# Kernel optimization log

Measured on AMD Instinct MI355X. Metric: run time of the kernel, lower is better.

## Reference

```python
import jax, jax.numpy as jnp
import numpy as np

B, R, C, OUT, IN = 256, 1152, 10, 16, 8


def setup_inputs() -> dict:
    key = jax.random.key(0)
    kx, kw = jax.random.split(key)
    x = jax.random.normal(kx, (B, R, IN), dtype=jnp.float32)
    W = jax.random.normal(kw, (R, C, OUT, IN), dtype=jnp.float32)
    return {"x": x, "W": W}


def _squash(s):
    # s: [B, C, OUT]
    mag_sq = jnp.sum(s * s, axis=-1, keepdims=True)
    mag = jnp.sqrt(mag_sq + 1e-8)
    return mag_sq / (1.0 + mag_sq) * (s / (mag + 1e-8))


def reference(x, W):
    # u_hat[b,r,c,o] = sum_i W[r,c,o,i] * x[b,r,i]  (no explicit W.repeat)
    u_hat = jnp.einsum('rcoi,bri->brco', W, x)
    b_ij = jnp.zeros((B, R, C), dtype=u_hat.dtype)
    v_j = None
    for it in range(3):
        c_ij = jax.nn.softmax(b_ij, axis=2)              # [B,R,C]
        s_j = jnp.einsum('brc,brco->bco', c_ij, u_hat)   # [B,C,OUT]
        v_j = _squash(s_j)                               # [B,C,OUT]
        if it < 2:
            b_ij = b_ij + jnp.einsum('brco,bco->brc', u_hat, v_j)
    return v_j
```

## Files before the change

kernel.cpp:

```cpp
#include <hip/hip_runtime.h>
#include <math.h>


typedef _Float16 h2 __attribute__((ext_vector_type(2)));
typedef _Float16 h4 __attribute__((ext_vector_type(4)));

#if __has_builtin(__builtin_amdgcn_fdot2)
#define FDOT2(a, b, c) __builtin_amdgcn_fdot2((a), (b), (c), false)
#else
static __device__ __forceinline__ float FDOT2(h2 a, h2 b, float c) {
    return c + (float)a.x * (float)b.x + (float)a.y * (float)b.y;
}
#endif

#if __has_builtin(__builtin_amdgcn_rcpf)
#define FRCP(x) __builtin_amdgcn_rcpf(x)
#else
#define FRCP(x) (1.0f / (x))
#endif

#define BCH2(u) __builtin_bit_cast(h2, (u))

template<int CTRL>
static __device__ __forceinline__ float dpp_xadd(float x) {
    const int t = __builtin_amdgcn_update_dpp(
        0, __builtin_bit_cast(int, x), CTRL, 0xF, 0xF, true);
    return x + __builtin_bit_cast(float, t);
}
static __device__ __forceinline__ float og_allsum(float l) {
    l = dpp_xadd<0xB1>(l);
    l = dpp_xadd<0x4E>(l);
    l = dpp_xadd<0x141>(l);
    return l;
}

namespace {
constexpr int Bdim = 256;
constexpr int Rdim = 1152;
constexpr int Cdim = 10;
constexpr int Odim = 16;
constexpr int Idim = 8;
constexpr int CO   = 160;

constexpr int Rpad  = 1280;
constexpr int RPC   = 10;
constexpr int NPAIR = 5;
constexpr int NCH   = 128;
constexpr int NSP   = 32;
constexpr int WROW  = Cdim * Odim * Idim;
}

__global__ __launch_bounds__(256)
void conv_wx(const float* __restrict__ W, const float* __restrict__ x,
             _Float16* __restrict__ W16, _Float16* __restrict__ X16)
{
    constexpr int NW4 = Rpad * WROW / 4;
    constexpr int NX4 = Rpad * Bdim * Idim / 4;
    const int i = blockIdx.x * 256 + threadIdx.x;
    if (i < NW4) {
        const int r = i / (WROW / 4);
        h4 o = { (_Float16)0.f, (_Float16)0.f, (_Float16)0.f, (_Float16)0.f };
        if (r < Rdim) {
            const float4 v = reinterpret_cast<const float4*>(W)[i];
            o = { (_Float16)v.x, (_Float16)v.y, (_Float16)v.z, (_Float16)v.w };
        }
        reinterpret_cast<h4*>(W16)[i] = o;
    } else if (i < NW4 + NX4) {
        const int j    = i - NW4;
        const int r    = j / (Bdim * 2);
        const int rem  = j - r * (Bdim * 2);
        const int b    = rem >> 1;
        const int half = rem & 1;
        h4 o = { (_Float16)0.f, (_Float16)0.f, (_Float16)0.f, (_Float16)0.f };
        if (r < Rdim) {
            const float4 v = reinterpret_cast<const float4*>(x)
                [((size_t)b * Rdim + r) * 2 + half];
            o = { (_Float16)v.x, (_Float16)v.y, (_Float16)v.z, (_Float16)v.w };
        }
        reinterpret_cast<h4*>(X16)[j] = o;
    }
}

__device__ __forceinline__ void stagepair(const _Float16* __restrict__ src,
                                          _Float16* dst, int lane)
{
#pragma unroll
    for (int k = 0; k < 5; ++k) {
        const _Float16* s = src + (size_t)(k * 64 + lane) * 8;
        _Float16* d = dst + k * 512;
        __builtin_amdgcn_global_load_lds((const __attribute__((address_space(1))) void*)s,
                                         (__attribute__((address_space(3))) void*)d,
                                         16, 0, 0);
    }
}

template<bool FIRST>
__global__ __launch_bounds__(256)
void caps_iter(const _Float16* __restrict__ X16, const _Float16* __restrict__ W16,
               const float* __restrict__ Vsum, float* __restrict__ s_part)
{
    __shared__ __align__(16) _Float16 Wstage[4][2][2560];

    const int tid  = threadIdx.x;
    const int wv   = tid >> 6;
    const int lane = tid & 63;
    const int og   = lane & 7;
    const int bl   = lane >> 3;

    const int quad   = blockIdx.x;
    const int bgroup = blockIdx.y;
    const int chunk  = quad * 4 + wv;
    const int r0     = chunk * RPC;
    const int b0     = bgroup * 16 + bl;
    const int b1     = b0 + 8;

    float va0[Cdim], vb0[Cdim], va1[Cdim], vb1[Cdim];
    if constexpr (!FIRST) {
#pragma unroll
        for (int c = 0; c < Cdim; ++c) {
            const float2 p = *reinterpret_cast<const float2*>(
                Vsum + (size_t)b0 * CO + c * Odim + og * 2);
            va0[c] = p.x; vb0[c] = p.y;
            const float2 q = *reinterpret_cast<const float2*>(
                Vsum + (size_t)b1 * CO + c * Odim + og * 2);
            va1[c] = q.x; vb1[c] = q.y;
        }
    }

    float sA0[Cdim], sA1[Cdim], sB0[Cdim], sB1[Cdim];
#pragma unroll
    for (int c = 0; c < Cdim; ++c) { sA0[c] = 0.f; sA1[c] = 0.f; sB0[c] = 0.f; sB1[c] = 0.f; }

    const _Float16* Wr = W16 + (size_t)r0 * WROW;
    _Float16* const st0 = &Wstage[wv][0][0];
    _Float16* const st1 = &Wstage[wv][1][0];

    stagepair(Wr, st0, lane);
    uint4 xA0, xA1, xB0, xB1;
    {
        const _Float16* xr0 = X16 + ((size_t)(r0 + 0) * Bdim) * Idim;
        const _Float16* xr1 = X16 + ((size_t)(r0 + 1) * Bdim) * Idim;
        xA0 = *reinterpret_cast<const uint4*>(xr0 + b0 * Idim);
        xB0 = *reinterpret_cast<const uint4*>(xr0 + b1 * Idim);
        xA1 = *reinterpret_cast<const uint4*>(xr1 + b0 * Idim);
        xB1 = *reinterpret_cast<const uint4*>(xr1 + b1 * Idim);
    }

    for (int p = 0; p < NPAIR; ++p) {
        asm volatile("s_waitcnt vmcnt(0)" ::: "memory");

        const _Float16* stcur = (p & 1) ? st1 : st0;
        _Float16* stnxt = (p & 1) ? st0 : st1;
        uint4 nA0, nA1, nB0, nB1;
        if (p + 1 < NPAIR) {
            stagepair(Wr + (size_t)(p + 1) * 2 * WROW, stnxt, lane);
            const int rn = r0 + (p + 1) * 2;
            const _Float16* xr0 = X16 + ((size_t)(rn + 0) * Bdim) * Idim;
            const _Float16* xr1 = X16 + ((size_t)(rn + 1) * Bdim) * Idim;
            nA0 = *reinterpret_cast<const uint4*>(xr0 + b0 * Idim);
            nB0 = *reinterpret_cast<const uint4*>(xr0 + b1 * Idim);
            nA1 = *reinterpret_cast<const uint4*>(xr1 + b0 * Idim);
            nB1 = *reinterpret_cast<const uint4*>(xr1 + b1 * Idim);
        }

#pragma unroll
        for (int rl = 0; rl < 2; ++rl) {
            const uint4 xva = rl ? xA1 : xA0;
            const uint4 xvb = rl ? xB1 : xB0;
            const h2 a0 = BCH2(xva.x), a1 = BCH2(xva.y), a2 = BCH2(xva.z), a3 = BCH2(xva.w);
            const h2 b0h = BCH2(xvb.x), b1h = BCH2(xvb.y), b2h = BCH2(xvb.z), b3h = BCH2(xvb.w);

            const _Float16* wbase = stcur + rl * WROW + og * 16;
            float uA0[Cdim], uA1[Cdim], uB0[Cdim], uB1[Cdim];
#pragma unroll
            for (int c = 0; c < Cdim; ++c) {
                const uint4* wp = reinterpret_cast<const uint4*>(wbase + c * (Odim * Idim));
                const uint4 w0 = wp[0], w1 = wp[1];
                float t;
                t = FDOT2(BCH2(w0.x), a0, 0.f);  t = FDOT2(BCH2(w0.y), a1, t);
                t = FDOT2(BCH2(w0.z), a2, t);    uA0[c] = FDOT2(BCH2(w0.w), a3, t);
                t = FDOT2(BCH2(w1.x), a0, 0.f);  t = FDOT2(BCH2(w1.y), a1, t);
                t = FDOT2(BCH2(w1.z), a2, t);    uA1[c] = FDOT2(BCH2(w1.w), a3, t);
                t = FDOT2(BCH2(w0.x), b0h, 0.f); t = FDOT2(BCH2(w0.y), b1h, t);
                t = FDOT2(BCH2(w0.z), b2h, t);   uB0[c] = FDOT2(BCH2(w0.w), b3h, t);
                t = FDOT2(BCH2(w1.x), b0h, 0.f); t = FDOT2(BCH2(w1.y), b1h, t);
                t = FDOT2(BCH2(w1.z), b2h, t);   uB1[c] = FDOT2(BCH2(w1.w), b3h, t);
            }

            if constexpr (FIRST) {
#pragma unroll
                for (int c = 0; c < Cdim; ++c) {
                    sA0[c] += 0.1f * uA0[c];  sA1[c] += 0.1f * uA1[c];
                    sB0[c] += 0.1f * uB0[c];  sB1[c] += 0.1f * uB1[c];
                }
            } else {
                float eA[Cdim], eB[Cdim];
                float sumA = 0.f, sumB = 0.f;
#pragma unroll
                for (int c = 0; c < Cdim; ++c) {
                    float lA = uA0[c] * va0[c] + uA1[c] * vb0[c];
                    lA = og_allsum(lA);
                    eA[c] = __expf(lA);  sumA += eA[c];
                    float lB = uB0[c] * va1[c] + uB1[c] * vb1[c];
                    lB = og_allsum(lB);
                    eB[c] = __expf(lB);  sumB += eB[c];
                }
                const float rA = FRCP(sumA), rB = FRCP(sumB);
#pragma unroll
                for (int c = 0; c < Cdim; ++c) {
                    const float cwA = eA[c] * rA;
                    sA0[c] += cwA * uA0[c];  sA1[c] += cwA * uA1[c];
                    const float cwB = eB[c] * rB;
                    sB0[c] += cwB * uB0[c];  sB1[c] += cwB * uB1[c];
                }
            }
        }

        if (p + 1 < NPAIR) { xA0 = nA0; xA1 = nA1; xB0 = nB0; xB1 = nB1; }
    }

    __syncthreads();
    float* red = reinterpret_cast<float*>(&Wstage[0][0][0]);
    {
        float* p0 = red + (wv * 16 + bl) * CO + og * 2;
        float* p1 = red + (wv * 16 + bl + 8) * CO + og * 2;
#pragma unroll
        for (int c = 0; c < Cdim; ++c) {
            *reinterpret_cast<float2*>(p0 + c * Odim) = make_float2(sA0[c], sA1[c]);
            *reinterpret_cast<float2*>(p1 + c * Odim) = make_float2(sB0[c], sB1[c]);
        }
    }
    __syncthreads();
#pragma unroll
    for (int k = 0; k < 10; ++k) {
        const int j = k * 256 + tid;
        const float t = red[j] + red[j + 2560] + red[j + 5120] + red[j + 7680];
        const int b2 = j / CO;
        const int co = j - b2 * CO;
        s_part[((size_t)quad * Bdim + bgroup * 16 + b2) * CO + co] = t;
    }
}

template<int MODE>
__global__ __launch_bounds__(256)
void caps_reduce(const float* __restrict__ s_part, float* __restrict__ Vsum,
                 float* __restrict__ out)
{
    const int idx = blockIdx.x * 256 + threadIdx.x;
    float s = 0.f;
#pragma unroll 8
    for (int k = 0; k < NSP; ++k) s += s_part[(size_t)k * (Bdim * CO) + idx];

    float ssq = s * s;
    ssq += __shfl_xor(ssq, 1);
    ssq += __shfl_xor(ssq, 2);
    ssq += __shfl_xor(ssq, 4);
    ssq += __shfl_xor(ssq, 8);

    const float mag = sqrtf(ssq + 1e-8f);
    const float v = ssq / (1.f + ssq) * s / (mag + 1e-8f);

    if constexpr (MODE == 2) out[idx] = v;
    else if constexpr (MODE == 1) Vsum[idx] += v;
    else Vsum[idx] = v;
}

extern "C" void kernel_launch(void* const* d_in, const int* in_sizes, int n_in,
                              void* d_out, int out_size, void* d_ws, size_t ws_size,
                              hipStream_t stream)
{
    const float* x = (const float*)d_in[0];
    const float* W = (const float*)d_in[1];
    float* out = (float*)d_out;

    float* s_part = (float*)d_ws;
    float* Vsum   = s_part + (size_t)NSP * Bdim * CO;
    _Float16* W16 = (_Float16*)(Vsum + Bdim * CO);
    _Float16* X16 = W16 + (size_t)Rpad * WROW;

    conv_wx<<<dim3(4160), dim3(256), 0, stream>>>(W, x, W16, X16);

    const dim3 gi(NSP, Bdim / 16);
    const dim3 bi(256);
    const dim3 gr((Bdim * CO) / 256);
    const dim3 br(256);

    caps_iter<true><<<gi, bi, 0, stream>>>(X16, W16, Vsum, s_part);
    caps_reduce<0><<<gr, br, 0, stream>>>(s_part, Vsum, out);
    caps_iter<false><<<gi, bi, 0, stream>>>(X16, W16, Vsum, s_part);
    caps_reduce<1><<<gr, br, 0, stream>>>(s_part, Vsum, out);
    caps_iter<false><<<gi, bi, 0, stream>>>(X16, W16, Vsum, s_part);
    caps_reduce<2><<<gr, br, 0, stream>>>(s_part, Vsum, out);
}
```

Before: 101.3 us.

## Triple-buffer W staging in LDS with prefetch distance two and partial waits

Each wave's LDS staging for W grows from two buffers to three. W tiles are now prefetched two row-pairs ahead, and the full vmcnt(0) drain becomes vmcnt(5), so the newest staging transfer can stay in flight during compute. The per-class LDS reads are also grouped into batches of five classes before the dot products, so more loads are outstanding at once. The cost is a larger LDS footprint per block (60 KB instead of 40 KB), which may limit how many blocks fit on each CU, and higher register pressure from the batched W registers.

```diff
diff --git a/kernel.cpp b/kernel.cpp
--- a/kernel.cpp
+++ b/kernel.cpp
@@ -45,7 +45,6 @@
 constexpr int Rpad  = 1280;
 constexpr int RPC   = 10;
 constexpr int NPAIR = 5;
-constexpr int NCH   = 128;
 constexpr int NSP   = 32;
 constexpr int WROW  = Cdim * Odim * Idim;
 }
@@ -99,7 +98,7 @@
 void caps_iter(const _Float16* __restrict__ X16, const _Float16* __restrict__ W16,
                const float* __restrict__ Vsum, float* __restrict__ s_part)
 {
-    __shared__ __align__(16) _Float16 Wstage[4][2][2560];
+    __shared__ __align__(16) _Float16 Wst[4][3][2560];
 
     const int tid  = threadIdx.x;
     const int wv   = tid >> 6;
@@ -107,12 +106,12 @@
     const int og   = lane & 7;
     const int bl   = lane >> 3;
 
-    const int quad   = blockIdx.x;
-    const int bgroup = blockIdx.y;
-    const int chunk  = quad * 4 + wv;
-    const int r0     = chunk * RPC;
-    const int b0     = bgroup * 16 + bl;
-    const int b1     = b0 + 8;
+    const int quad = blockIdx.x;
+    const int bgrp = blockIdx.y;
+    const int chunk = quad * 4 + wv;
+    const int r0    = chunk * RPC;
+    const int b0    = bgrp * 16 + bl;
+    const int b1    = b0 + 8;
 
     float va0[Cdim], vb0[Cdim], va1[Cdim], vb1[Cdim];
     if constexpr (!FIRST) {
@@ -129,62 +128,73 @@
 
     float sA0[Cdim], sA1[Cdim], sB0[Cdim], sB1[Cdim];
 #pragma unroll
-    for (int c = 0; c < Cdim; ++c) { sA0[c] = 0.f; sA1[c] = 0.f; sB0[c] = 0.f; sB1[c] = 0.f; }
+    for (int c = 0; c < Cdim; ++c) { sA0[c]=0.f; sA1[c]=0.f; sB0[c]=0.f; sB1[c]=0.f; }
 
     const _Float16* Wr = W16 + (size_t)r0 * WROW;
-    _Float16* const st0 = &Wstage[wv][0][0];
-    _Float16* const st1 = &Wstage[wv][1][0];
-
-    stagepair(Wr, st0, lane);
-    uint4 xA0, xA1, xB0, xB1;
+
+    stagepair(Wr, &Wst[wv][0][0], lane);
+    uint4 xc0, xc1, xc2, xc3;
     {
-        const _Float16* xr0 = X16 + ((size_t)(r0 + 0) * Bdim) * Idim;
-        const _Float16* xr1 = X16 + ((size_t)(r0 + 1) * Bdim) * Idim;
-        xA0 = *reinterpret_cast<const uint4*>(xr0 + b0 * Idim);
-        xB0 = *reinterpret_cast<const uint4*>(xr0 + b1 * Idim);
-        xA1 = *reinterpret_cast<const uint4*>(xr1 + b0 * Idim);
-        xB1 = *reinterpret_cast<const uint4*>(xr1 + b1 * Idim);
-    }
+        const _Float16* xr = X16 + (size_t)r0 * (Bdim * Idim);
+        xc0 = *reinterpret_cast<const uint4*>(xr + b0 * Idim);
+        xc1 = *reinterpret_cast<const uint4*>(xr + b1 * Idim);
+        xc2 = *reinterpret_cast<const uint4*>(xr + (Bdim * Idim) + b0 * Idim);
+        xc3 = *reinterpret_cast<const uint4*>(xr + (Bdim * Idim) + b1 * Idim);
+    }
+    stagepair(Wr + 2 * WROW, &Wst[wv][1][0], lane);
 
     for (int p = 0; p < NPAIR; ++p) {
-        asm volatile("s_waitcnt vmcnt(0)" ::: "memory");
-
-        const _Float16* stcur = (p & 1) ? st1 : st0;
-        _Float16* stnxt = (p & 1) ? st0 : st1;
-        uint4 nA0, nA1, nB0, nB1;
+        if (p + 1 < NPAIR)
+            asm volatile("s_waitcnt vmcnt(5)" ::: "memory");
+        else
+            asm volatile("s_waitcnt vmcnt(0)" ::: "memory");
+
+        const _Float16* stcur = &Wst[wv][p % 3][0];
+
+        uint4 xn0, xn1, xn2, xn3;
         if (p + 1 < NPAIR) {
-            stagepair(Wr + (size_t)(p + 1) * 2 * WROW, stnxt, lane);
-            const int rn = r0 + (p + 1) * 2;
-            const _Float16* xr0 = X16 + ((size_t)(rn + 0) * Bdim) * Idim;
-            const _Float16* xr1 = X16 + ((size_t)(rn + 1) * Bdim) * Idim;
-            nA0 = *reinterpret_cast<const uint4*>(xr0 + b0 * Idim);
-            nB0 = *reinterpret_cast<const uint4*>(xr0 + b1 * Idim);
-            nA1 = *reinterpret_cast<const uint4*>(xr1 + b0 * Idim);
-            nB1 = *reinterpret_cast<const uint4*>(xr1 + b1 * Idim);
-        }
+            const _Float16* xr = X16 + (size_t)(r0 + (p + 1) * 2) * (Bdim * Idim);
+            xn0 = *reinterpret_cast<const uint4*>(xr + b0 * Idim);
+            xn1 = *reinterpret_cast<const uint4*>(xr + b1 * Idim);
+            xn2 = *reinterpret_cast<const uint4*>(xr + (Bdim * Idim) + b0 * Idim);
+            xn3 = *reinterpret_cast<const uint4*>(xr + (Bdim * Idim) + b1 * Idim);
+        }
+        if (p + 2 < NPAIR)
+            stagepair(Wr + (size_t)(p + 2) * 2 * WROW, &Wst[wv][(p + 2) % 3][0], lane);
 
 #pragma unroll
         for (int rl = 0; rl < 2; ++rl) {
-            const uint4 xva = rl ? xA1 : xA0;
-            const uint4 xvb = rl ? xB1 : xB0;
+            const uint4 xva = rl ? xc2 : xc0;
+            const uint4 xvb = rl ? xc3 : xc1;
             const h2 a0 = BCH2(xva.x), a1 = BCH2(xva.y), a2 = BCH2(xva.z), a3 = BCH2(xva.w);
-            const h2 b0h = BCH2(xvb.x), b1h = BCH2(xvb.y), b2h = BCH2(xvb.z), b3h = BCH2(xvb.w);
+            const h2 e0 = BCH2(xvb.x), e1 = BCH2(xvb.y), e2 = BCH2(xvb.z), e3 = BCH2(xvb.w);
 
             const _Float16* wbase = stcur + rl * WROW + og * 16;
             float uA0[Cdim], uA1[Cdim], uB0[Cdim], uB1[Cdim];
 #pragma unroll
-            for (int c = 0; c < Cdim; ++c) {
-                const uint4* wp = reinterpret_cast<const uint4*>(wbase + c * (Odim * Idim));
-                const uint4 w0 = wp[0], w1 = wp[1];
-                float t;
-                t = FDOT2(BCH2(w0.x), a0, 0.f);  t = FDOT2(BCH2(w0.y), a1, t);
-                t = FDOT2(BCH2(w0.z), a2, t);    uA0[c] = FDOT2(BCH2(w0.w), a3, t);
-                t = FDOT2(BCH2(w1.x), a0, 0.f);  t = FDOT2(BCH2(w1.y), a1, t);
-                t = FDOT2(BCH2(w1.z), a2, t);    uA1[c] = FDOT2(BCH2(w1.w), a3, t);
-                t = FDOT2(BCH2(w0.x), b0h, 0.f); t = FDOT2(BCH2(w0.y), b1h, t);
-                t = FDOT2(BCH2(w0.z), b2h, t);   uB0[c] = FDOT2(BCH2(w0.w), b3h, t);
-                t = FDOT2(BCH2(w1.x), b0h, 0.f); t = FDOT2(BCH2(w1.y), b1h, t);
-                t = FDOT2(BCH2(w1.z), b2h, t);   uB1[c] = FDOT2(BCH2(w1.w), b3h, t);
+            for (int g = 0; g < 2; ++g) {
+                uint4 wreg[10];
+#pragma unroll
+                for (int c5 = 0; c5 < 5; ++c5) {
+                    const uint4* wp = reinterpret_cast<const uint4*>(
+                        wbase + (g * 5 + c5) * (Odim * Idim));
+                    wreg[2 * c5]     = wp[0];
+                    wreg[2 * c5 + 1] = wp[1];
+                }
+#pragma unroll
+                for (int c5 = 0; c5 < 5; ++c5) {
+                    const int c = g * 5 + c5;
+                    const uint4 w0 = wreg[2 * c5], w1 = wreg[2 * c5 + 1];
+                    float t;
+                    t = FDOT2(BCH2(w0.x), a0, 0.f);  t = FDOT2(BCH2(w0.y), a1, t);
+                    t = FDOT2(BCH2(w0.z), a2, t);    uA0[c] = FDOT2(BCH2(w0.w), a3, t);
+                    t = FDOT2(BCH2(w1.x), a0, 0.f);  t = FDOT2(BCH2(w1.y), a1, t);
+                    t = FDOT2(BCH2(w1.z), a2, t);    uA1[c] = FDOT2(BCH2(w1.w), a3, t);
+                    t = FDOT2(BCH2(w0.x), e0, 0.f);  t = FDOT2(BCH2(w0.y), e1, t);
+                    t = FDOT2(BCH2(w0.z), e2, t);    uB0[c] = FDOT2(BCH2(w0.w), e3, t);
+                    t = FDOT2(BCH2(w1.x), e0, 0.f);  t = FDOT2(BCH2(w1.y), e1, t);
+                    t = FDOT2(BCH2(w1.z), e2, t);    uB1[c] = FDOT2(BCH2(w1.w), e3, t);
+                }
             }
 
             if constexpr (FIRST) {
@@ -216,11 +226,11 @@
             }
         }
 
-        if (p + 1 < NPAIR) { xA0 = nA0; xA1 = nA1; xB0 = nB0; xB1 = nB1; }
+        if (p + 1 < NPAIR) { xc0 = xn0; xc1 = xn1; xc2 = xn2; xc3 = xn3; }
     }
 
     __syncthreads();
-    float* red = reinterpret_cast<float*>(&Wstage[0][0][0]);
+    float* red = reinterpret_cast<float*>(&Wst[0][0][0]);
     {
         float* p0 = red + (wv * 16 + bl) * CO + og * 2;
         float* p1 = red + (wv * 16 + bl + 8) * CO + og * 2;
@@ -237,7 +247,7 @@
         const float t = red[j] + red[j + 2560] + red[j + 5120] + red[j + 7680];
         const int b2 = j / CO;
         const int co = j - b2 * CO;
-        s_part[((size_t)quad * Bdim + bgroup * 16 + b2) * CO + co] = t;
+        s_part[((size_t)quad * Bdim + bgrp * 16 + b2) * CO + co] = t;
     }
 }
 
```

Result: no change. 100.3 us (-1.0%).
